# Kernel tuning notes

Measured on AMD Instinct MI355X. Metric: run time of the kernel, lower is better.

The kernel has to match this reference:

```python
import jax, jax.numpy as jnp
import numpy as np

N_NODES = 50000
N_EDGES = 500000
D_FEAT = 128


def setup_inputs() -> dict:
    key = jax.random.key(0)
    k1, k2, k3 = jax.random.split(key, 3)
    r = jax.random.normal(k1, (N_NODES, D_FEAT), dtype=jnp.float32)
    e = jax.random.normal(k2, (N_EDGES, D_FEAT), dtype=jnp.float32)
    a = jax.random.randint(k3, (N_EDGES, 2), 0, N_NODES, dtype=jnp.int64)
    return {"r": r, "e": e, "a": a}


def reference(r, e, a):
    # message: gather source/target node features along edges, scale by edge feats
    rij = r[a[:, 0]] * e  # [E, D] messages src -> dst
    rji = r[a[:, 1]] * e  # [E, D] messages dst -> src
    # aggregate: scatter_add into node dimension (fixed num_segments for jit)
    out = jax.ops.segment_sum(rij, a[:, 1], num_segments=r.shape[0])
    out = out + jax.ops.segment_sum(rji, a[:, 0], num_segments=r.shape[0])
    return out  # [N, D]
```

## Files before the change

kernel.cpp:

```cpp
#include <hip/hip_runtime.h>
#include <hip/hip_fp16.h>


#define D_FEAT 128
#define SCAN_TILE 1024
#define CHUNK 4096
#define G_GRP 8

typedef float vf2 __attribute__((ext_vector_type(2)));

__device__ inline unsigned pack_h2(float a, float b) {
    __half2 h;
    h.x = __float2half_rn(a);
    h.y = __float2half_rn(b);
    return *reinterpret_cast<unsigned*>(&h);
}
__device__ inline float2 unpack_h2(unsigned u) {
    __half2 h = *reinterpret_cast<__half2*>(&u);
    return __half22float2(h);
}

__global__ __launch_bounds__(256) void hist1_kernel(
    const int* __restrict__ a, const float* __restrict__ r,
    unsigned* __restrict__ ghist, uint2* __restrict__ r16,
    int n_entries, int nwords, int n_r4) {
    extern __shared__ unsigned h[];
    for (int i = threadIdx.x; i < nwords; i += blockDim.x) h[i] = 0u;
    __syncthreads();
    int s = blockIdx.x * CHUNK;
    int e = s + CHUNK;
    if (e > n_entries) e = n_entries;
    for (int idx = s + threadIdx.x; idx < e; idx += blockDim.x) {
        int n = a[idx];
        atomicAdd(&h[n >> 2], 1u << ((n & 3) * 8));
    }
    __syncthreads();
    unsigned* dst = ghist + (size_t)blockIdx.x * nwords;
    for (int i = threadIdx.x; i < nwords; i += blockDim.x) dst[i] = h[i];
    int tid = blockIdx.x * blockDim.x + threadIdx.x;
    int nth = gridDim.x * blockDim.x;
    for (int i = tid; i < n_r4; i += nth) {
        const float4 v = ((const float4*)r)[i];
        uint2 p;
        p.x = pack_h2(v.x, v.y);
        p.y = pack_h2(v.z, v.w);
        r16[i] = p;
    }
}

__global__ void m2a_kernel(const unsigned* __restrict__ ghist,
                           unsigned char* __restrict__ base,
                           unsigned char* __restrict__ gsum,
                           int n_nodes, int nblk, int gblk, int nwords) {
    int n = blockIdx.x * blockDim.x + threadIdx.x;
    if (n >= n_nodes) return;
    int g = blockIdx.y;
    int b0 = g * gblk;
    int b1 = b0 + gblk;
    if (b1 > nblk) b1 = nblk;
    int w = n >> 2, sh = (n & 3) * 8;
    int run = 0;
    for (int b = b0; b < b1; ++b) {
        base[(size_t)b * n_nodes + n] = (unsigned char)run;
        run += (int)((ghist[(size_t)b * nwords + w] >> sh) & 0xffu);
    }
    gsum[(size_t)g * n_nodes + n] = (unsigned char)run;
}

__global__ void m2b_kernel(const unsigned char* __restrict__ gsum,
                           unsigned char* __restrict__ gbase,
                           int* __restrict__ deg, int n_nodes) {
    int n = blockIdx.x * blockDim.x + threadIdx.x;
    if (n >= n_nodes) return;
    int run = 0;
    #pragma unroll
    for (int g = 0; g < G_GRP; ++g) {
        gbase[(size_t)g * n_nodes + n] = (unsigned char)run;
        run += (int)gsum[(size_t)g * n_nodes + n];
    }
    deg[n] = run;
}

__global__ void scanA_kernel(const int* __restrict__ deg, int* __restrict__ bsum,
                             int n) {
    __shared__ int wsum[16];
    int t = threadIdx.x, lane = t & 63, w = t >> 6;
    int i = blockIdx.x * SCAN_TILE + t;
    int v = (i < n) ? deg[i] : 0;
    #pragma unroll
    for (int off = 32; off > 0; off >>= 1) v += __shfl_down(v, off, 64);
    if (lane == 0) wsum[w] = v;
    __syncthreads();
    if (t == 0) {
        int s = 0;
        #pragma unroll
        for (int k = 0; k < 16; ++k) s += wsum[k];
        bsum[blockIdx.x] = s;
    }
}

__global__ void scanB_kernel(int* __restrict__ bsum, int* __restrict__ bbase,
                             int* __restrict__ offs, int nblk, int n) {
    if (threadIdx.x == 0) {
        int run = 0;
        for (int b = 0; b < nblk; ++b) {
            bbase[b] = run;
            run += bsum[b];
        }
        offs[n] = run;
    }
}

__global__ void scanC_kernel(const int* __restrict__ deg, int* __restrict__ offs,
                             const int* __restrict__ bbase, int n) {
    __shared__ int wsum[16];
    int t = threadIdx.x, lane = t & 63, w = t >> 6;
    int i = blockIdx.x * SCAN_TILE + t;
    int v = (i < n) ? deg[i] : 0;
    int x = v;
    #pragma unroll
    for (int off = 1; off < 64; off <<= 1) {
        int y = __shfl_up(x, off, 64);
        if (lane >= off) x += y;
    }
    if (lane == 63) wsum[w] = x;
    __syncthreads();
    if (w == 0 && lane < 16) {
        int s = wsum[lane];
        #pragma unroll
        for (int off = 1; off < 16; off <<= 1) {
            int y = __shfl_up(s, off, 64);
            if (lane >= off) s += y;
        }
        wsum[lane] = s;
    }
    __syncthreads();
    int wbase = (w == 0) ? 0 : wsum[w - 1];
    if (i < n) offs[i] = x - v + wbase + bbase[blockIdx.x];
}

__global__ __launch_bounds__(256) void fill3_kernel(
    const int* __restrict__ a, const int* __restrict__ offs,
    const unsigned char* __restrict__ base,
    const unsigned char* __restrict__ gbase, int2* __restrict__ pl,
    int n_entries, int n_nodes, int nwords, int gblk) {
    extern __shared__ unsigned cur[];
    for (int i = threadIdx.x; i < nwords; i += blockDim.x) cur[i] = 0u;
    __syncthreads();
    int s = blockIdx.x * CHUNK;
    int e = s + CHUNK;
    if (e > n_entries) e = n_entries;
    const unsigned char* brow = base + (size_t)blockIdx.x * n_nodes;
    const unsigned char* grow = gbase + (size_t)(blockIdx.x / gblk) * n_nodes;
    for (int idx = s + threadIdx.x; idx < e; idx += blockDim.x) {
        int other  = a[idx];
        int center = a[idx ^ 1];
        int sh = (center & 3) * 8;
        unsigned old = atomicAdd(&cur[center >> 2], 1u << sh);
        int local = (int)((old >> sh) & 0xffu);
        int pos = offs[center] + (int)grow[center] + (int)brow[center] + local;
        pl[pos] = make_int2(idx >> 1, other);
    }
}

__global__ __launch_bounds__(256) void gather_nt_kernel(
    const unsigned* __restrict__ r16, const float* __restrict__ e,
    const int* __restrict__ offs, const int2* __restrict__ pl,
    float* __restrict__ out, int n_nodes) {
    int n = blockIdx.x * 4 + (threadIdx.x >> 6);
    if (n >= n_nodes) return;
    int lane = threadIdx.x & 63;
    int start = offs[n];
    int end = offs[n + 1];
    float accx = 0.f, accy = 0.f;
    int i = start;
    for (; i + 4 <= end; i += 4) {
        unsigned long long w0 = __builtin_nontemporal_load(
            (const unsigned long long*)(pl + i));
        unsigned long long w1 = __builtin_nontemporal_load(
            (const unsigned long long*)(pl + i + 1));
        unsigned long long w2 = __builtin_nontemporal_load(
            (const unsigned long long*)(pl + i + 2));
        unsigned long long w3 = __builtin_nontemporal_load(
            (const unsigned long long*)(pl + i + 3));
        int e0i = (int)(unsigned)w0, o0 = (int)(w0 >> 32);
        int e1i = (int)(unsigned)w1, o1 = (int)(w1 >> 32);
        int e2i = (int)(unsigned)w2, o2 = (int)(w2 >> 32);
        int e3i = (int)(unsigned)w3, o3 = (int)(w3 >> 32);
        vf2 ev0 = __builtin_nontemporal_load(
            ((const vf2*)(e + (size_t)e0i * D_FEAT)) + lane);
        vf2 ev1 = __builtin_nontemporal_load(
            ((const vf2*)(e + (size_t)e1i * D_FEAT)) + lane);
        vf2 ev2 = __builtin_nontemporal_load(
            ((const vf2*)(e + (size_t)e2i * D_FEAT)) + lane);
        vf2 ev3 = __builtin_nontemporal_load(
            ((const vf2*)(e + (size_t)e3i * D_FEAT)) + lane);
        float2 r0 = unpack_h2(r16[(size_t)o0 * 64 + lane]);
        float2 r1 = unpack_h2(r16[(size_t)o1 * 64 + lane]);
        float2 r2 = unpack_h2(r16[(size_t)o2 * 64 + lane]);
        float2 r3 = unpack_h2(r16[(size_t)o3 * 64 + lane]);
        accx += ev0.x * r0.x; accy += ev0.y * r0.y;
        accx += ev1.x * r1.x; accy += ev1.y * r1.y;
        accx += ev2.x * r2.x; accy += ev2.y * r2.y;
        accx += ev3.x * r3.x; accy += ev3.y * r3.y;
    }
    for (; i < end; ++i) {
        unsigned long long w0 = __builtin_nontemporal_load(
            (const unsigned long long*)(pl + i));
        int e0i = (int)(unsigned)w0, o0 = (int)(w0 >> 32);
        vf2 ev0 = __builtin_nontemporal_load(
            ((const vf2*)(e + (size_t)e0i * D_FEAT)) + lane);
        float2 r0 = unpack_h2(r16[(size_t)o0 * 64 + lane]);
        accx += ev0.x * r0.x; accy += ev0.y * r0.y;
    }
    float2 res;
    res.x = accx;
    res.y = accy;
    *((float2*)(out + (size_t)n * D_FEAT) + lane) = res;
}


__global__ void hist_kernel(const int* __restrict__ a, int* __restrict__ deg,
                            int n_elems) {
    int i = blockIdx.x * blockDim.x + threadIdx.x;
    if (i < n_elems) atomicAdd(&deg[a[i]], 1);
}

__global__ void fill_kernel(const int* __restrict__ a, int* __restrict__ cursor,
                            int2* __restrict__ pl, int n_entries) {
    int k = blockIdx.x * blockDim.x + threadIdx.x;
    if (k >= n_entries) return;
    int edge = k >> 1, j = k & 1;
    int other  = a[2 * edge + j];
    int center = a[2 * edge + (j ^ 1)];
    int pos = atomicAdd(&cursor[center], 1);
    pl[pos] = make_int2(edge, other);
}

__global__ void scanC_cursor_kernel(int* __restrict__ deg, int* __restrict__ offs,
                                    const int* __restrict__ bbase, int n) {
    __shared__ int wsum[16];
    int t = threadIdx.x, lane = t & 63, w = t >> 6;
    int i = blockIdx.x * SCAN_TILE + t;
    int v = (i < n) ? deg[i] : 0;
    int x = v;
    #pragma unroll
    for (int off = 1; off < 64; off <<= 1) {
        int y = __shfl_up(x, off, 64);
        if (lane >= off) x += y;
    }
    if (lane == 63) wsum[w] = x;
    __syncthreads();
    if (w == 0 && lane < 16) {
        int s = wsum[lane];
        #pragma unroll
        for (int off = 1; off < 16; off <<= 1) {
            int y = __shfl_up(s, off, 64);
            if (lane >= off) s += y;
        }
        wsum[lane] = s;
    }
    __syncthreads();
    int wbase = (w == 0) ? 0 : wsum[w - 1];
    if (i < n) {
        int excl = x - v + wbase + bbase[blockIdx.x];
        offs[i] = excl;
        deg[i] = excl;
    }
}

__global__ __launch_bounds__(256) void gather_f32_kernel(
    const float* __restrict__ r, const float* __restrict__ e,
    const int* __restrict__ offs, const int2* __restrict__ pl,
    float* __restrict__ out, int n_nodes) {
    int n = blockIdx.x * 4 + (threadIdx.x >> 6);
    if (n >= n_nodes) return;
    int lane = threadIdx.x & 63;
    int start = offs[n];
    int end = offs[n + 1];
    float accx = 0.f, accy = 0.f;
    for (int i = start; i < end; ++i) {
        int2 p0 = pl[i];
        float2 ev0 = *((const float2*)(e + (size_t)p0.x * D_FEAT) + lane);
        float2 rv0 = *((const float2*)(r + (size_t)p0.y * D_FEAT) + lane);
        accx += ev0.x * rv0.x;
        accy += ev0.y * rv0.y;
    }
    float2 res;
    res.x = accx;
    res.y = accy;
    *((float2*)(out + (size_t)n * D_FEAT) + lane) = res;
}

__global__ void mp_scatter_kernel(const float* __restrict__ r,
                                  const float* __restrict__ e,
                                  const int* __restrict__ a,
                                  float* __restrict__ out,
                                  int n_edges) {
    long long gid = (long long)blockIdx.x * blockDim.x + threadIdx.x;
    int edge = (int)(gid >> 7);
    int feat = (int)(gid & 127);
    if (edge >= n_edges) return;
    int s = a[2 * edge];
    int d = a[2 * edge + 1];
    float ev = e[(long long)edge * D_FEAT + feat];
    float rs = r[(long long)s * D_FEAT + feat];
    float rd = r[(long long)d * D_FEAT + feat];
    atomicAdd(&out[(long long)d * D_FEAT + feat], rs * ev);
    atomicAdd(&out[(long long)s * D_FEAT + feat], rd * ev);
}

extern "C" void kernel_launch(void* const* d_in, const int* in_sizes, int n_in,
                              void* d_out, int out_size, void* d_ws, size_t ws_size,
                              hipStream_t stream) {
    const float* r = (const float*)d_in[0];
    const float* e = (const float*)d_in[1];
    const int*   a = (const int*)d_in[2];
    float* out = (float*)d_out;
    (void)n_in;

    int n_nodes   = in_sizes[0] / D_FEAT;
    int n_edges   = in_sizes[1] / D_FEAT;
    int n_entries = 2 * n_edges;
    int n_r4      = in_sizes[0] / 4;

    int block = 256;
    int grid_e = (n_entries + block - 1) / block;
    int nblk_scan = (n_nodes + SCAN_TILE - 1) / SCAN_TILE;
    int nblk_c = (n_entries + CHUNK - 1) / CHUNK;
    int gblk   = (nblk_c + G_GRP - 1) / G_GRP;
    int nwords = (n_nodes + 3) / 4;
    size_t lds_bytes = (size_t)nwords * sizeof(unsigned);

    {
        size_t ghist_words = (size_t)nblk_c * nwords;
        size_t base_bytes  = (((size_t)nblk_c * n_nodes) + 3) & ~(size_t)3;
        size_t gsum_bytes  = (((size_t)G_GRP * n_nodes) + 3) & ~(size_t)3;
        size_t ints_tail   = (size_t)n_nodes + (size_t)(n_nodes + 1)
                           + 2 * (size_t)nblk_scan;
        size_t head_bytes  = ghist_words * 4 + base_bytes + 2 * gsum_bytes
                           + (size_t)n_r4 * sizeof(uint2) + ints_tail * 4;
        head_bytes = (head_bytes + 7) & ~(size_t)7;
        size_t need = head_bytes + (size_t)n_entries * sizeof(int2);
        if (ws_size >= need && nblk_scan <= 1024 && lds_bytes <= 64 * 1024) {
            unsigned*      ghist = (unsigned*)d_ws;
            unsigned char* basep = (unsigned char*)(ghist + ghist_words);
            unsigned char* gsum  = basep + base_bytes;
            unsigned char* gbase = gsum + gsum_bytes;
            uint2*         r16   = (uint2*)(gbase + gsum_bytes);
            int*           deg   = (int*)(r16 + n_r4);
            int*           offs  = deg + n_nodes;
            int*           bsum  = offs + n_nodes + 1;
            int*           bbase = bsum + nblk_scan;
            int2*          pl    = (int2*)((char*)d_ws + head_bytes);

            hist1_kernel<<<nblk_c, block, lds_bytes, stream>>>(
                a, r, ghist, r16, n_entries, nwords, n_r4);
            dim3 gm2a((n_nodes + block - 1) / block, G_GRP);
            m2a_kernel<<<gm2a, block, 0, stream>>>(ghist, basep, gsum,
                                                   n_nodes, nblk_c, gblk,
                                                   nwords);
            int grid_m = (n_nodes + block - 1) / block;
            m2b_kernel<<<grid_m, block, 0, stream>>>(gsum, gbase, deg, n_nodes);
            scanA_kernel<<<nblk_scan, SCAN_TILE, 0, stream>>>(deg, bsum,
                                                              n_nodes);
            scanB_kernel<<<1, 64, 0, stream>>>(bsum, bbase, offs, nblk_scan,
                                               n_nodes);
            scanC_kernel<<<nblk_scan, SCAN_TILE, 0, stream>>>(deg, offs, bbase,
                                                              n_nodes);
            fill3_kernel<<<nblk_c, block, lds_bytes, stream>>>(
                a, offs, basep, gbase, pl, n_entries, n_nodes, nwords, gblk);
            int grid_g = (n_nodes + 3) / 4;
            gather_nt_kernel<<<grid_g, 256, 0, stream>>>(
                (const unsigned*)r16, e, offs, pl, out, n_nodes);
            return;
        }
    }

    {
        size_t ints_head = (size_t)n_nodes + (size_t)(n_nodes + 1)
                         + 2 * (size_t)nblk_scan;
        ints_head = (ints_head + 1) & ~(size_t)1;
        size_t need = ints_head * sizeof(int) + (size_t)n_entries * sizeof(int2);
        if (ws_size >= need && nblk_scan <= 1024) {
            int*  deg  = (int*)d_ws;
            int*  offs = deg + n_nodes;
            int*  bsum = offs + n_nodes + 1;
            int*  bbase= bsum + nblk_scan;
            int2* pl   = (int2*)((int*)d_ws + ints_head);

            hipMemsetAsync(deg, 0, (size_t)n_nodes * sizeof(int), stream);
            hist_kernel<<<grid_e, block, 0, stream>>>(a, deg, n_entries);
            scanA_kernel<<<nblk_scan, SCAN_TILE, 0, stream>>>(deg, bsum, n_nodes);
            scanB_kernel<<<1, 64, 0, stream>>>(bsum, bbase, offs, nblk_scan,
                                               n_nodes);
            scanC_cursor_kernel<<<nblk_scan, SCAN_TILE, 0, stream>>>(deg, offs,
                                                                     bbase,
                                                                     n_nodes);
            fill_kernel<<<grid_e, block, 0, stream>>>(a, deg, pl, n_entries);
            int grid_g = (n_nodes + 3) / 4;
            gather_f32_kernel<<<grid_g, 256, 0, stream>>>(r, e, offs, pl, out,
                                                          n_nodes);
            return;
        }
    }

    hipMemsetAsync(d_out, 0, (size_t)out_size * sizeof(float), stream);
    long long total = (long long)n_edges * D_FEAT;
    long long grid = (total + block - 1) / block;
    mp_scatter_kernel<<<(int)grid, block, 0, stream>>>(r, e, a, out, n_edges);
}
```

Baseline: 499.4 us.

## Split wave into half-wave edge pairs with 16B loads, move fp16 pack, double chunk

The gather kernel now processes two edges at once per wave, with each 32-lane half taking one edge and loading 16-byte vectors of edge features and 8-byte packed fp16 node rows. The halves are combined with a cross-half shuffle before a nontemporal 16-byte store. The fp16 conversion of r moves from the histogram kernel into the m2a kernel. The histogram chunk size is doubled, which halves the number of per-block histograms. The aim is wider memory transactions and more loads in flight per wave, at the cost of a shuffle reduction and an idle half wave on odd edge tails.

```diff
diff --git a/kernel.cpp b/kernel.cpp
--- a/kernel.cpp
+++ b/kernel.cpp
@@ -4,10 +4,12 @@
 
 #define D_FEAT 128
 #define SCAN_TILE 1024
-#define CHUNK 4096
+#define CHUNK 8192
 #define G_GRP 8
 
 typedef float vf2 __attribute__((ext_vector_type(2)));
+typedef float vf4 __attribute__((ext_vector_type(4)));
+typedef unsigned long long ull_t;
 
 __device__ inline unsigned pack_h2(float a, float b) {
     __half2 h;
@@ -21,9 +23,8 @@
 }
 
 __global__ __launch_bounds__(256) void hist1_kernel(
-    const int* __restrict__ a, const float* __restrict__ r,
-    unsigned* __restrict__ ghist, uint2* __restrict__ r16,
-    int n_entries, int nwords, int n_r4) {
+    const int* __restrict__ a, unsigned* __restrict__ ghist,
+    int n_entries, int nwords) {
     extern __shared__ unsigned h[];
     for (int i = threadIdx.x; i < nwords; i += blockDim.x) h[i] = 0u;
     __syncthreads();
@@ -37,8 +38,31 @@
     __syncthreads();
     unsigned* dst = ghist + (size_t)blockIdx.x * nwords;
     for (int i = threadIdx.x; i < nwords; i += blockDim.x) dst[i] = h[i];
-    int tid = blockIdx.x * blockDim.x + threadIdx.x;
-    int nth = gridDim.x * blockDim.x;
+}
+
+__global__ void m2a_kernel(const unsigned* __restrict__ ghist,
+                           const float* __restrict__ r,
+                           unsigned char* __restrict__ base,
+                           unsigned char* __restrict__ gsum,
+                           uint2* __restrict__ r16,
+                           int n_nodes, int nblk, int gblk, int nwords,
+                           int n_r4) {
+    int n = blockIdx.x * blockDim.x + threadIdx.x;
+    if (n < n_nodes) {
+        int g = blockIdx.y;
+        int b0 = g * gblk;
+        int b1 = b0 + gblk;
+        if (b1 > nblk) b1 = nblk;
+        int w = n >> 2, sh = (n & 3) * 8;
+        int run = 0;
+        for (int b = b0; b < b1; ++b) {
+            base[(size_t)b * n_nodes + n] = (unsigned char)run;
+            run += (int)((ghist[(size_t)b * nwords + w] >> sh) & 0xffu);
+        }
+        gsum[(size_t)blockIdx.y * n_nodes + n] = (unsigned char)run;
+    }
+    int tid = (blockIdx.y * gridDim.x + blockIdx.x) * blockDim.x + threadIdx.x;
+    int nth = gridDim.x * gridDim.y * blockDim.x;
     for (int i = tid; i < n_r4; i += nth) {
         const float4 v = ((const float4*)r)[i];
         uint2 p;
@@ -46,25 +70,6 @@
         p.y = pack_h2(v.z, v.w);
         r16[i] = p;
     }
-}
-
-__global__ void m2a_kernel(const unsigned* __restrict__ ghist,
-                           unsigned char* __restrict__ base,
-                           unsigned char* __restrict__ gsum,
-                           int n_nodes, int nblk, int gblk, int nwords) {
-    int n = blockIdx.x * blockDim.x + threadIdx.x;
-    if (n >= n_nodes) return;
-    int g = blockIdx.y;
-    int b0 = g * gblk;
-    int b1 = b0 + gblk;
-    if (b1 > nblk) b1 = nblk;
-    int w = n >> 2, sh = (n & 3) * 8;
-    int run = 0;
-    for (int b = b0; b < b1; ++b) {
-        base[(size_t)b * n_nodes + n] = (unsigned char)run;
-        run += (int)((ghist[(size_t)b * nwords + w] >> sh) & 0xffu);
-    }
-    gsum[(size_t)g * n_nodes + n] = (unsigned char)run;
 }
 
 __global__ void m2b_kernel(const unsigned char* __restrict__ gsum,
@@ -163,60 +168,65 @@
     }
 }
 
-__global__ __launch_bounds__(256) void gather_nt_kernel(
+__global__ __launch_bounds__(256) void gather_w2_kernel(
     const unsigned* __restrict__ r16, const float* __restrict__ e,
     const int* __restrict__ offs, const int2* __restrict__ pl,
     float* __restrict__ out, int n_nodes) {
     int n = blockIdx.x * 4 + (threadIdx.x >> 6);
     if (n >= n_nodes) return;
     int lane = threadIdx.x & 63;
+    int half = lane >> 5;
+    int l32  = lane & 31;
     int start = offs[n];
     int end = offs[n + 1];
-    float accx = 0.f, accy = 0.f;
+    float ax = 0.f, ay = 0.f, az = 0.f, aw = 0.f;
     int i = start;
-    for (; i + 4 <= end; i += 4) {
-        unsigned long long w0 = __builtin_nontemporal_load(
-            (const unsigned long long*)(pl + i));
-        unsigned long long w1 = __builtin_nontemporal_load(
-            (const unsigned long long*)(pl + i + 1));
-        unsigned long long w2 = __builtin_nontemporal_load(
-            (const unsigned long long*)(pl + i + 2));
-        unsigned long long w3 = __builtin_nontemporal_load(
-            (const unsigned long long*)(pl + i + 3));
-        int e0i = (int)(unsigned)w0, o0 = (int)(w0 >> 32);
-        int e1i = (int)(unsigned)w1, o1 = (int)(w1 >> 32);
-        int e2i = (int)(unsigned)w2, o2 = (int)(w2 >> 32);
-        int e3i = (int)(unsigned)w3, o3 = (int)(w3 >> 32);
-        vf2 ev0 = __builtin_nontemporal_load(
-            ((const vf2*)(e + (size_t)e0i * D_FEAT)) + lane);
-        vf2 ev1 = __builtin_nontemporal_load(
-            ((const vf2*)(e + (size_t)e1i * D_FEAT)) + lane);
-        vf2 ev2 = __builtin_nontemporal_load(
-            ((const vf2*)(e + (size_t)e2i * D_FEAT)) + lane);
-        vf2 ev3 = __builtin_nontemporal_load(
-            ((const vf2*)(e + (size_t)e3i * D_FEAT)) + lane);
-        float2 r0 = unpack_h2(r16[(size_t)o0 * 64 + lane]);
-        float2 r1 = unpack_h2(r16[(size_t)o1 * 64 + lane]);
-        float2 r2 = unpack_h2(r16[(size_t)o2 * 64 + lane]);
-        float2 r3 = unpack_h2(r16[(size_t)o3 * 64 + lane]);
-        accx += ev0.x * r0.x; accy += ev0.y * r0.y;
-        accx += ev1.x * r1.x; accy += ev1.y * r1.y;
-        accx += ev2.x * r2.x; accy += ev2.y * r2.y;
-        accx += ev3.x * r3.x; accy += ev3.y * r3.y;
-    }
-    for (; i < end; ++i) {
-        unsigned long long w0 = __builtin_nontemporal_load(
-            (const unsigned long long*)(pl + i));
-        int e0i = (int)(unsigned)w0, o0 = (int)(w0 >> 32);
-        vf2 ev0 = __builtin_nontemporal_load(
-            ((const vf2*)(e + (size_t)e0i * D_FEAT)) + lane);
-        float2 r0 = unpack_h2(r16[(size_t)o0 * 64 + lane]);
-        accx += ev0.x * r0.x; accy += ev0.y * r0.y;
-    }
-    float2 res;
-    res.x = accx;
-    res.y = accy;
-    *((float2*)(out + (size_t)n * D_FEAT) + lane) = res;
+    #define PAIR_STEP(OFS)                                                    \
+        {                                                                     \
+            ull_t w = __builtin_nontemporal_load(                             \
+                (const ull_t*)(pl + i + (OFS) + half));                       \
+            int ei = (int)(unsigned)w;                                        \
+            int oi = (int)(w >> 32);                                          \
+            vf4 ev = __builtin_nontemporal_load(                              \
+                ((const vf4*)(e + (size_t)ei * D_FEAT)) + l32);               \
+            uint2 ru = *(((const uint2*)(r16 + (size_t)oi * 64)) + l32);      \
+            float2 rlo = unpack_h2(ru.x);                                     \
+            float2 rhi = unpack_h2(ru.y);                                     \
+            ax += ev.x * rlo.x; ay += ev.y * rlo.y;                           \
+            az += ev.z * rhi.x; aw += ev.w * rhi.y;                           \
+        }
+    for (; i + 8 <= end; i += 8) {
+        PAIR_STEP(0)
+        PAIR_STEP(2)
+        PAIR_STEP(4)
+        PAIR_STEP(6)
+    }
+    for (; i + 2 <= end; i += 2) {
+        PAIR_STEP(0)
+    }
+    if (i < end && half == 0) {
+        ull_t w = __builtin_nontemporal_load((const ull_t*)(pl + i));
+        int ei = (int)(unsigned)w;
+        int oi = (int)(w >> 32);
+        vf4 ev = __builtin_nontemporal_load(
+            ((const vf4*)(e + (size_t)ei * D_FEAT)) + l32);
+        uint2 ru = *(((const uint2*)(r16 + (size_t)oi * 64)) + l32);
+        float2 rlo = unpack_h2(ru.x);
+        float2 rhi = unpack_h2(ru.y);
+        ax += ev.x * rlo.x; ay += ev.y * rlo.y;
+        az += ev.z * rhi.x; aw += ev.w * rhi.y;
+    }
+    #undef PAIR_STEP
+    ax += __shfl_xor(ax, 32);
+    ay += __shfl_xor(ay, 32);
+    az += __shfl_xor(az, 32);
+    aw += __shfl_xor(aw, 32);
+    if (half == 0) {
+        vf4 res;
+        res.x = ax; res.y = ay; res.z = az; res.w = aw;
+        __builtin_nontemporal_store(
+            res, ((vf4*)(out + (size_t)n * D_FEAT)) + l32);
+    }
 }
 
 
@@ -354,12 +364,13 @@
             int*           bbase = bsum + nblk_scan;
             int2*          pl    = (int2*)((char*)d_ws + head_bytes);
 
-            hist1_kernel<<<nblk_c, block, lds_bytes, stream>>>(
-                a, r, ghist, r16, n_entries, nwords, n_r4);
+            hist1_kernel<<<nblk_c, block, lds_bytes, stream>>>(a, ghist,
+                                                               n_entries,
+                                                               nwords);
             dim3 gm2a((n_nodes + block - 1) / block, G_GRP);
-            m2a_kernel<<<gm2a, block, 0, stream>>>(ghist, basep, gsum,
+            m2a_kernel<<<gm2a, block, 0, stream>>>(ghist, r, basep, gsum, r16,
                                                    n_nodes, nblk_c, gblk,
-                                                   nwords);
+                                                   nwords, n_r4);
             int grid_m = (n_nodes + block - 1) / block;
             m2b_kernel<<<grid_m, block, 0, stream>>>(gsum, gbase, deg, n_nodes);
             scanA_kernel<<<nblk_scan, SCAN_TILE, 0, stream>>>(deg, bsum,
@@ -371,7 +382,7 @@
             fill3_kernel<<<nblk_c, block, lds_bytes, stream>>>(
                 a, offs, basep, gbase, pl, n_entries, n_nodes, nwords, gblk);
             int grid_g = (n_nodes + 3) / 4;
-            gather_nt_kernel<<<grid_g, 256, 0, stream>>>(
+            gather_w2_kernel<<<grid_g, 256, 0, stream>>>(
                 (const unsigned*)r16, e, offs, pl, out, n_nodes);
             return;
         }
```

After: 496.3 us. About the same (-0.6%).
